# Optimization experiments

Measured on AMD Instinct MI355X. Metric: run time of the kernel, lower is better.

The kernel has to match this reference:

```python
import jax, jax.numpy as jnp
import numpy as np

ENTITY_SIZE = 100000
RELATION_SIZE = 500
DIM = 128
BATCH = 8192
MARGIN = 1.0


def _xavier_normal(key, shape):
    fan_in, fan_out = shape[1], shape[0]
    std = float(np.sqrt(2.0 / (fan_in + fan_out)))
    return jax.random.normal(key, shape, dtype=jnp.float32) * std


def setup_inputs() -> dict:
    key = jax.random.key(0)
    k1, k2, k3, k4, k5 = jax.random.split(key, 5)
    entities = _xavier_normal(k1, (ENTITY_SIZE, DIM))
    relations = _xavier_normal(k2, (RELATION_SIZE, DIM))
    transfer_matrix = _xavier_normal(k3, (RELATION_SIZE, DIM * DIM))
    positive_triples = jax.random.randint(k4, (BATCH, 3), 0, RELATION_SIZE, dtype=jnp.int32).astype(jnp.int64)
    negative_triples = jax.random.randint(k5, (BATCH, 3), 0, RELATION_SIZE, dtype=jnp.int32).astype(jnp.int64)
    return {
        "positive_triples": positive_triples,
        "negative_triples": negative_triples,
        "entities": entities,
        "relations": relations,
        "transfer_matrix": transfer_matrix,
    }


def _l2_normalize(x, eps=1e-12):
    # matches F.normalize(x, 2, -1): x / max(||x||_2, eps)
    n = jnp.linalg.norm(x, ord=2, axis=-1, keepdims=True)
    return x / jnp.maximum(n, eps)


def _calc_score(triples, entities, relations, transfer_matrix):
    heads, rels, tails = triples[:, 0], triples[:, 1], triples[:, 2]
    h = entities[heads]                      # [B, D]
    r = relations[rels]                      # [B, D]
    t = entities[tails]                      # [B, D]
    Mr = transfer_matrix[rels].reshape(-1, DIM, DIM)  # [B, D, D]
    # per-relation transfer: row-vector times matrix
    h = jnp.einsum('bd,bde->be', h, Mr)
    t = jnp.einsum('bd,bde->be', t, Mr)
    h = _l2_normalize(h)
    r = _l2_normalize(r)
    t = _l2_normalize(t)
    return jnp.sum(jnp.abs(h + r - t), axis=-1)  # L1 norm per triple, [B]


def reference(positive_triples, negative_triples, entities, relations, transfer_matrix):
    pos = _calc_score(positive_triples, entities, relations, transfer_matrix)
    neg = _calc_score(negative_triples, entities, relations, transfer_matrix)
    # MarginRankingLoss(margin=1.0) with target = -1:
    # mean(max(0, -y*(pos - neg) + margin)) = mean(relu(pos - neg + margin))
    return jnp.mean(jax.nn.relu(pos - neg + MARGIN))
```

## Files before the change

### kernel.cpp

```cpp
#include <hip/hip_runtime.h>
#include <math.h>

#define DIM 128
#define BATCH 8192
#define NTRIP (2 * BATCH)
#define NREL 500
#define MARGIN 1.0f
#define CAP 96
#define BSTR 136

typedef __attribute__((ext_vector_type(8))) short short8;
typedef __attribute__((ext_vector_type(4))) short short4v;
typedef __attribute__((ext_vector_type(4))) float f32x4;

__device__ __forceinline__ float wave_sum(float v) {
    v += __shfl_xor(v, 32, 64);
    v += __shfl_xor(v, 16, 64);
    v += __shfl_xor(v, 8, 64);
    v += __shfl_xor(v, 4, 64);
    v += __shfl_xor(v, 2, 64);
    v += __shfl_xor(v, 1, 64);
    return v;
}

__device__ __forceinline__ float quad_sum(float v) {
    v += __shfl_xor(v, 1, 64);
    v += __shfl_xor(v, 2, 64);
    v += __shfl_xor(v, 4, 64);
    v += __shfl_xor(v, 8, 64);
    return v;
}

__device__ __forceinline__ short f2bf(float f) {
    unsigned u = __float_as_uint(f);
    u = (u + 0x7fffu + ((u >> 16) & 1u)) >> 16;
    return (short)u;
}

__global__ __launch_bounds__(256)
void transr_bucket(const int* __restrict__ pos, const int* __restrict__ neg,
                   int* __restrict__ rel_count, int2* __restrict__ ht,
                   int* __restrict__ ids) {
    const int gid = blockIdx.x * 256 + threadIdx.x;
    const int* trip = (gid < BATCH) ? (pos + gid * 3) : (neg + (gid - BATCH) * 3);
    const int h = trip[0], r = trip[1], t = trip[2];
    const int slot = atomicAdd(&rel_count[r], 1);
    if (slot < CAP) {
        ht[r * CAP + slot] = make_int2(h, t);
        ids[r * CAP + slot] = gid;
    }
}

__global__ __launch_bounds__(512)
void transr_main(const float* __restrict__ entities,
                 const float* __restrict__ relations,
                 const float* __restrict__ transfer,
                 const int* __restrict__ rel_count,
                 const int2* __restrict__ ht, const int* __restrict__ ids,
                 float* __restrict__ scores) {
    __shared__ __align__(16) short Bt[DIM * BSTR];
    __shared__ float rhat_s[DIM];

    const int rel = blockIdx.x;
    const int tid = threadIdx.x;
    const int cnt = min(rel_count[rel], CAP);

    const int lane = tid & 63;
    const int w = tid >> 6;
    const int n = lane & 15;
    const int q = lane >> 4;
    const int jm = n >> 1;
    const int sel = n & 1;

    if (tid < DIM) rhat_s[tid] = relations[(size_t)rel * DIM + tid];

    const int2* __restrict__ ht_rel = ht + rel * CAP;
    const int* __restrict__ ids_rel = ids + rel * CAP;
    const int ntiles = (cnt + 7) >> 3;
    int2 pair0 = make_int2(0, 0);
    if (w < ntiles && cnt > 0) pair0 = ht_rel[min(w * 8 + jm, cnt - 1)];

    const float4* __restrict__ mrf4 = (const float4*)(transfer + (size_t)rel * (DIM * DIM));
    const int m = tid & 31;
    const int g = tid >> 5;
    const int n0 = m * 4;
#pragma unroll
    for (int it = 0; it < 2; ++it) {
        const int f0 = it * 2048 + g * 128 + m;
        const float4 v0 = mrf4[f0];
        const float4 v1 = mrf4[f0 + 32];
        const float4 v2 = mrf4[f0 + 64];
        const float4 v3 = mrf4[f0 + 96];
        const int k0 = it * 64 + g * 4;
        const float* p0 = (const float*)&v0;
        const float* p1 = (const float*)&v1;
        const float* p2 = (const float*)&v2;
        const float* p3 = (const float*)&v3;
#pragma unroll
        for (int j = 0; j < 4; ++j) {
            short4v wv;
            wv[0] = f2bf(p0[j]);
            wv[1] = f2bf(p1[j]);
            wv[2] = f2bf(p2[j]);
            wv[3] = f2bf(p3[j]);
            *(short4v*)(&Bt[(n0 + j) * BSTR + k0]) = wv;
        }
    }
    __syncthreads();

    const float a0 = rhat_s[lane], b0 = rhat_s[lane + 64];
    const float ssr = wave_sum(fmaf(a0, a0, b0 * b0));
    const float rinv = 1.0f / fmaxf(sqrtf(ssr), 1e-12f);

    float r_reg[8];
#pragma unroll
    for (int nt = 0; nt < 8; ++nt) r_reg[nt] = rhat_s[nt * 16 + n] * rinv;

    for (int tile = w; tile < ntiles; tile += 8) {
        const int2 pair = (tile == w) ? pair0 : ht_rel[min(tile * 8 + jm, cnt - 1)];
        const float* __restrict__ erow = entities + (size_t)(sel ? pair.y : pair.x) * DIM;

        short8 af[4];
#pragma unroll
        for (int kc = 0; kc < 4; ++kc) {
            const float4 u0 = *(const float4*)(erow + kc * 32 + q * 8);
            const float4 u1 = *(const float4*)(erow + kc * 32 + q * 8 + 4);
            short8 a;
            a[0] = f2bf(u0.x); a[1] = f2bf(u0.y); a[2] = f2bf(u0.z); a[3] = f2bf(u0.w);
            a[4] = f2bf(u1.x); a[5] = f2bf(u1.y); a[6] = f2bf(u1.z); a[7] = f2bf(u1.w);
            af[kc] = a;
        }

        f32x4 acc[8];
#pragma unroll
        for (int nt = 0; nt < 8; ++nt) acc[nt] = (f32x4){0.0f, 0.0f, 0.0f, 0.0f};
#pragma unroll
        for (int nt = 0; nt < 8; ++nt) {
            const short* __restrict__ bp = &Bt[(nt * 16 + n) * BSTR + q * 8];
#pragma unroll
            for (int kc = 0; kc < 4; ++kc) {
                const short8 bfr = *(const short8*)(bp + kc * 32);
                acc[nt] = __builtin_amdgcn_mfma_f32_16x16x32_bf16(af[kc], bfr, acc[nt], 0, 0, 0);
            }
        }

#pragma unroll
        for (int p = 0; p < 4; p += 2) {
            float hs = 0.0f, ts = 0.0f;
#pragma unroll
            for (int nt = 0; nt < 8; ++nt) {
                hs = fmaf(acc[nt][p], acc[nt][p], hs);
                ts = fmaf(acc[nt][p + 1], acc[nt][p + 1], ts);
            }
            hs = quad_sum(hs);
            ts = quad_sum(ts);
            const float invh = 1.0f / fmaxf(sqrtf(hs), 1e-12f);
            const float invt = 1.0f / fmaxf(sqrtf(ts), 1e-12f);
            float ss = 0.0f;
#pragma unroll
            for (int nt = 0; nt < 8; ++nt)
                ss += fabsf(fmaf(acc[nt][p], invh, r_reg[nt]) - acc[nt][p + 1] * invt);
            ss = quad_sum(ss);
            if (n == 0) {
                const int jS = min(tile * 8 + (q * 2 + (p >> 1)), cnt - 1);
                scores[ids_rel[jS]] = ss;
            }
        }
    }
}

__global__ __launch_bounds__(512)
void transr_loss(const float* __restrict__ scores, float* __restrict__ out) {
    const int tid = threadIdx.x;
    float s = 0.0f;
#pragma unroll
    for (int it = 0; it < 4; ++it) {
        const int i = it * 512 + tid;
        const float4 a = ((const float4*)scores)[i];
        const float4 b = ((const float4*)(scores + BATCH))[i];
        float d;
        d = a.x - b.x + MARGIN; s += (d > 0.0f) ? d : 0.0f;
        d = a.y - b.y + MARGIN; s += (d > 0.0f) ? d : 0.0f;
        d = a.z - b.z + MARGIN; s += (d > 0.0f) ? d : 0.0f;
        d = a.w - b.w + MARGIN; s += (d > 0.0f) ? d : 0.0f;
    }
    s = wave_sum(s);
    __shared__ float red[8];
    if ((tid & 63) == 0) red[tid >> 6] = s;
    __syncthreads();
    if (tid == 0) {
        float t = 0.0f;
#pragma unroll
        for (int i = 0; i < 8; ++i) t += red[i];
        out[0] = t * (1.0f / (float)BATCH);
    }
}

extern "C" void kernel_launch(void* const* d_in, const int* in_sizes, int n_in,
                              void* d_out, int out_size, void* d_ws, size_t ws_size,
                              hipStream_t stream) {
    const int*   pos       = (const int*)d_in[0];
    const int*   neg       = (const int*)d_in[1];
    const float* entities  = (const float*)d_in[2];
    const float* relations = (const float*)d_in[3];
    const float* transfer  = (const float*)d_in[4];
    float* out = (float*)d_out;

    int*   wsi       = (int*)d_ws;
    float* scores    = (float*)d_ws;
    int*   rel_count = wsi + 16384;
    int*   ids       = wsi + 16896;
    int2*  ht        = (int2*)(wsi + 65536);

    hipMemsetAsync(rel_count, 0, NREL * sizeof(int), stream);
    transr_bucket<<<NTRIP / 256, 256, 0, stream>>>(pos, neg, rel_count, ht, ids);
    transr_main<<<NREL, 512, 0, stream>>>(entities, relations, transfer, rel_count,
                                          ht, ids, scores);
    transr_loss<<<1, 512, 0, stream>>>(scores, out);
}
```

Before: 124.7 us.

## Fuse relation bucketing into main kernel and swizzle transfer-matrix LDS layout

Drops the memset and the separate bucket kernel. Each relation block now scans all 16384 triples itself and gathers its matching head/tail/id lists into shared memory with LDS atomics. The transposed transfer matrix in LDS moves from a padded stride to an XOR-swizzled unpadded layout to avoid bank conflicts. This removes two launches and global atomics, but every block redundantly reads all triple indices (about 200 KB per block, served mostly from L2).

```diff
diff --git a/kernel.cpp b/kernel.cpp
--- a/kernel.cpp
+++ b/kernel.cpp
@@ -6,8 +6,7 @@
 #define NTRIP (2 * BATCH)
 #define NREL 500
 #define MARGIN 1.0f
-#define CAP 96
-#define BSTR 136
+#define CAPL 128
 
 typedef __attribute__((ext_vector_type(8))) short short8;
 typedef __attribute__((ext_vector_type(4))) short short4v;
@@ -37,34 +36,19 @@
     return (short)u;
 }
 
-__global__ __launch_bounds__(256)
-void transr_bucket(const int* __restrict__ pos, const int* __restrict__ neg,
-                   int* __restrict__ rel_count, int2* __restrict__ ht,
-                   int* __restrict__ ids) {
-    const int gid = blockIdx.x * 256 + threadIdx.x;
-    const int* trip = (gid < BATCH) ? (pos + gid * 3) : (neg + (gid - BATCH) * 3);
-    const int h = trip[0], r = trip[1], t = trip[2];
-    const int slot = atomicAdd(&rel_count[r], 1);
-    if (slot < CAP) {
-        ht[r * CAP + slot] = make_int2(h, t);
-        ids[r * CAP + slot] = gid;
-    }
-}
-
 __global__ __launch_bounds__(512)
-void transr_main(const float* __restrict__ entities,
+void transr_main(const int* __restrict__ pos, const int* __restrict__ neg,
+                 const float* __restrict__ entities,
                  const float* __restrict__ relations,
                  const float* __restrict__ transfer,
-                 const int* __restrict__ rel_count,
-                 const int2* __restrict__ ht, const int* __restrict__ ids,
                  float* __restrict__ scores) {
-    __shared__ __align__(16) short Bt[DIM * BSTR];
+    __shared__ __align__(16) short Bt[DIM * DIM];
     __shared__ float rhat_s[DIM];
+    __shared__ int lh[CAPL], lt[CAPL], lid[CAPL];
+    __shared__ int lcnt;
 
     const int rel = blockIdx.x;
     const int tid = threadIdx.x;
-    const int cnt = min(rel_count[rel], CAP);
-
     const int lane = tid & 63;
     const int w = tid >> 6;
     const int n = lane & 15;
@@ -72,13 +56,9 @@
     const int jm = n >> 1;
     const int sel = n & 1;
 
+    if (tid == 0) lcnt = 0;
     if (tid < DIM) rhat_s[tid] = relations[(size_t)rel * DIM + tid];
-
-    const int2* __restrict__ ht_rel = ht + rel * CAP;
-    const int* __restrict__ ids_rel = ids + rel * CAP;
-    const int ntiles = (cnt + 7) >> 3;
-    int2 pair0 = make_int2(0, 0);
-    if (w < ntiles && cnt > 0) pair0 = ht_rel[min(w * 8 + jm, cnt - 1)];
+    __syncthreads();
 
     const float4* __restrict__ mrf4 = (const float4*)(transfer + (size_t)rel * (DIM * DIM));
     const int m = tid & 31;
@@ -92,21 +72,42 @@
         const float4 v2 = mrf4[f0 + 64];
         const float4 v3 = mrf4[f0 + 96];
         const int k0 = it * 64 + g * 4;
+        const int u = k0 >> 3;
+        const int klo = k0 & 7;
         const float* p0 = (const float*)&v0;
         const float* p1 = (const float*)&v1;
         const float* p2 = (const float*)&v2;
         const float* p3 = (const float*)&v3;
 #pragma unroll
         for (int j = 0; j < 4; ++j) {
+            const int col = n0 + j;
             short4v wv;
             wv[0] = f2bf(p0[j]);
             wv[1] = f2bf(p1[j]);
             wv[2] = f2bf(p2[j]);
             wv[3] = f2bf(p3[j]);
-            *(short4v*)(&Bt[(n0 + j) * BSTR + k0]) = wv;
+            const int up = u ^ ((col >> 1) & 7);
+            *(short4v*)(&Bt[col * DIM + up * 8 + klo]) = wv;
+        }
+    }
+
+#pragma unroll 4
+    for (int it = 0; it < 32; ++it) {
+        const int gid = it * 512 + tid;
+        const int* __restrict__ t3 =
+            (it < 16) ? (pos + gid * 3) : (neg + (gid - BATCH) * 3);
+        const int h = t3[0];
+        const int r = t3[1];
+        const int t = t3[2];
+        if (r == rel) {
+            const int s = atomicAdd(&lcnt, 1);
+            if (s < CAPL) { lh[s] = h; lt[s] = t; lid[s] = gid; }
         }
     }
     __syncthreads();
+
+    const int cnt = min(lcnt, CAPL);
+    if (cnt == 0) return;
 
     const float a0 = rhat_s[lane], b0 = rhat_s[lane + 64];
     const float ssr = wave_sum(fmaf(a0, a0, b0 * b0));
@@ -116,9 +117,12 @@
 #pragma unroll
     for (int nt = 0; nt < 8; ++nt) r_reg[nt] = rhat_s[nt * 16 + n] * rinv;
 
+    const int ntiles = (cnt + 7) >> 3;
+    const int fcol = n >> 1;
     for (int tile = w; tile < ntiles; tile += 8) {
-        const int2 pair = (tile == w) ? pair0 : ht_rel[min(tile * 8 + jm, cnt - 1)];
-        const float* __restrict__ erow = entities + (size_t)(sel ? pair.y : pair.x) * DIM;
+        const int j = min(tile * 8 + jm, cnt - 1);
+        const int eid = sel ? lt[j] : lh[j];
+        const float* __restrict__ erow = entities + (size_t)eid * DIM;
 
         short8 af[4];
 #pragma unroll
@@ -136,10 +140,10 @@
         for (int nt = 0; nt < 8; ++nt) acc[nt] = (f32x4){0.0f, 0.0f, 0.0f, 0.0f};
 #pragma unroll
         for (int nt = 0; nt < 8; ++nt) {
-            const short* __restrict__ bp = &Bt[(nt * 16 + n) * BSTR + q * 8];
+            const short* __restrict__ bp = &Bt[(nt * 16 + n) * DIM];
 #pragma unroll
             for (int kc = 0; kc < 4; ++kc) {
-                const short8 bfr = *(const short8*)(bp + kc * 32);
+                const short8 bfr = *(const short8*)(bp + (((kc * 4 + q) ^ fcol) << 3));
                 acc[nt] = __builtin_amdgcn_mfma_f32_16x16x32_bf16(af[kc], bfr, acc[nt], 0, 0, 0);
             }
         }
@@ -163,7 +167,7 @@
             ss = quad_sum(ss);
             if (n == 0) {
                 const int jS = min(tile * 8 + (q * 2 + (p >> 1)), cnt - 1);
-                scores[ids_rel[jS]] = ss;
+                scores[lid[jS]] = ss;
             }
         }
     }
@@ -206,15 +210,9 @@
     const float* transfer  = (const float*)d_in[4];
     float* out = (float*)d_out;
 
-    int*   wsi       = (int*)d_ws;
-    float* scores    = (float*)d_ws;
-    int*   rel_count = wsi + 16384;
-    int*   ids       = wsi + 16896;
-    int2*  ht        = (int2*)(wsi + 65536);
-
-    hipMemsetAsync(rel_count, 0, NREL * sizeof(int), stream);
-    transr_bucket<<<NTRIP / 256, 256, 0, stream>>>(pos, neg, rel_count, ht, ids);
-    transr_main<<<NREL, 512, 0, stream>>>(entities, relations, transfer, rel_count,
-                                          ht, ids, scores);
+    float* scores = (float*)d_ws;
+
+    transr_main<<<NREL, 512, 0, stream>>>(pos, neg, entities, relations, transfer,
+                                          scores);
     transr_loss<<<1, 512, 0, stream>>>(scores, out);
 }
```

Result: slower. 134.5 us (+7.8%).

## Fuse loss reduction into main kernel, swizzle LDS B tile, hoist first entity load

Applied to the files above, without the earlier changes.

The final margin-loss reduction moves into the main kernel: the last block, found through an atomic done counter, computes the mean, which removes a separate launch. The padded LDS layout for the transfer matrix becomes an XOR-swizzled unpadded layout to avoid bank conflicts and save LDS. The first tile's entity rows are loaded before the barrier so the loads overlap with staging the B matrix. Launch bounds now request 4 blocks per CU, which may force register spills.

```diff
diff --git a/kernel.cpp b/kernel.cpp
--- a/kernel.cpp
+++ b/kernel.cpp
@@ -7,7 +7,6 @@
 #define NREL 500
 #define MARGIN 1.0f
 #define CAP 96
-#define BSTR 136
 
 typedef __attribute__((ext_vector_type(8))) short short8;
 typedef __attribute__((ext_vector_type(4))) short short4v;
@@ -51,15 +50,18 @@
     }
 }
 
-__global__ __launch_bounds__(512)
+__global__ __launch_bounds__(512, 4)
 void transr_main(const float* __restrict__ entities,
                  const float* __restrict__ relations,
                  const float* __restrict__ transfer,
                  const int* __restrict__ rel_count,
                  const int2* __restrict__ ht, const int* __restrict__ ids,
-                 float* __restrict__ scores) {
-    __shared__ __align__(16) short Bt[DIM * BSTR];
+                 float* __restrict__ scores, int* __restrict__ done,
+                 float* __restrict__ out) {
+    __shared__ __align__(16) short Bt[DIM * DIM];
     __shared__ float rhat_s[DIM];
+    __shared__ float red[8];
+    __shared__ int is_last;
 
     const int rel = blockIdx.x;
     const int tid = threadIdx.x;
@@ -92,107 +94,140 @@
         const float4 v2 = mrf4[f0 + 64];
         const float4 v3 = mrf4[f0 + 96];
         const int k0 = it * 64 + g * 4;
+        const int u = k0 >> 3;
+        const int klo = k0 & 7;
         const float* p0 = (const float*)&v0;
         const float* p1 = (const float*)&v1;
         const float* p2 = (const float*)&v2;
         const float* p3 = (const float*)&v3;
 #pragma unroll
         for (int j = 0; j < 4; ++j) {
+            const int col = n0 + j;
             short4v wv;
             wv[0] = f2bf(p0[j]);
             wv[1] = f2bf(p1[j]);
             wv[2] = f2bf(p2[j]);
             wv[3] = f2bf(p3[j]);
-            *(short4v*)(&Bt[(n0 + j) * BSTR + k0]) = wv;
-        }
-    }
-    __syncthreads();
-
-    const float a0 = rhat_s[lane], b0 = rhat_s[lane + 64];
-    const float ssr = wave_sum(fmaf(a0, a0, b0 * b0));
-    const float rinv = 1.0f / fmaxf(sqrtf(ssr), 1e-12f);
-
-    float r_reg[8];
-#pragma unroll
-    for (int nt = 0; nt < 8; ++nt) r_reg[nt] = rhat_s[nt * 16 + n] * rinv;
-
-    for (int tile = w; tile < ntiles; tile += 8) {
-        const int2 pair = (tile == w) ? pair0 : ht_rel[min(tile * 8 + jm, cnt - 1)];
-        const float* __restrict__ erow = entities + (size_t)(sel ? pair.y : pair.x) * DIM;
-
-        short8 af[4];
+            const int up = u ^ ((col >> 1) & 7);
+            *(short4v*)(&Bt[col * DIM + up * 8 + klo]) = wv;
+        }
+    }
+
+    short8 af0[4];
+    {
+        const float* __restrict__ erow0 =
+            entities + (size_t)(sel ? pair0.y : pair0.x) * DIM;
 #pragma unroll
         for (int kc = 0; kc < 4; ++kc) {
-            const float4 u0 = *(const float4*)(erow + kc * 32 + q * 8);
-            const float4 u1 = *(const float4*)(erow + kc * 32 + q * 8 + 4);
+            const float4 u0 = *(const float4*)(erow0 + kc * 32 + q * 8);
+            const float4 u1 = *(const float4*)(erow0 + kc * 32 + q * 8 + 4);
             short8 a;
             a[0] = f2bf(u0.x); a[1] = f2bf(u0.y); a[2] = f2bf(u0.z); a[3] = f2bf(u0.w);
             a[4] = f2bf(u1.x); a[5] = f2bf(u1.y); a[6] = f2bf(u1.z); a[7] = f2bf(u1.w);
-            af[kc] = a;
-        }
-
-        f32x4 acc[8];
-#pragma unroll
-        for (int nt = 0; nt < 8; ++nt) acc[nt] = (f32x4){0.0f, 0.0f, 0.0f, 0.0f};
-#pragma unroll
-        for (int nt = 0; nt < 8; ++nt) {
-            const short* __restrict__ bp = &Bt[(nt * 16 + n) * BSTR + q * 8];
-#pragma unroll
-            for (int kc = 0; kc < 4; ++kc) {
-                const short8 bfr = *(const short8*)(bp + kc * 32);
-                acc[nt] = __builtin_amdgcn_mfma_f32_16x16x32_bf16(af[kc], bfr, acc[nt], 0, 0, 0);
+            af0[kc] = a;
+        }
+    }
+    __syncthreads();
+
+    if (cnt > 0) {
+        const float a0 = rhat_s[lane], b0 = rhat_s[lane + 64];
+        const float ssr = wave_sum(fmaf(a0, a0, b0 * b0));
+        const float rinv = 1.0f / fmaxf(sqrtf(ssr), 1e-12f);
+
+        float r_reg[8];
+#pragma unroll
+        for (int nt = 0; nt < 8; ++nt) r_reg[nt] = rhat_s[nt * 16 + n] * rinv;
+
+        const int fcol = n >> 1;
+        for (int tile = w; tile < ntiles; tile += 8) {
+            short8 af[4];
+            if (tile == w) {
+#pragma unroll
+                for (int kc = 0; kc < 4; ++kc) af[kc] = af0[kc];
+            } else {
+                const int j = min(tile * 8 + jm, cnt - 1);
+                const int2 pair = ht_rel[j];
+                const float* __restrict__ erow =
+                    entities + (size_t)(sel ? pair.y : pair.x) * DIM;
+#pragma unroll
+                for (int kc = 0; kc < 4; ++kc) {
+                    const float4 u0 = *(const float4*)(erow + kc * 32 + q * 8);
+                    const float4 u1 = *(const float4*)(erow + kc * 32 + q * 8 + 4);
+                    short8 a;
+                    a[0] = f2bf(u0.x); a[1] = f2bf(u0.y); a[2] = f2bf(u0.z); a[3] = f2bf(u0.w);
+                    a[4] = f2bf(u1.x); a[5] = f2bf(u1.y); a[6] = f2bf(u1.z); a[7] = f2bf(u1.w);
+                    af[kc] = a;
+                }
             }
-        }
-
-#pragma unroll
-        for (int p = 0; p < 4; p += 2) {
-            float hs = 0.0f, ts = 0.0f;
+
+            f32x4 acc[8];
+#pragma unroll
+            for (int nt = 0; nt < 8; ++nt) acc[nt] = (f32x4){0.0f, 0.0f, 0.0f, 0.0f};
 #pragma unroll
             for (int nt = 0; nt < 8; ++nt) {
-                hs = fmaf(acc[nt][p], acc[nt][p], hs);
-                ts = fmaf(acc[nt][p + 1], acc[nt][p + 1], ts);
+                const short* __restrict__ bp = &Bt[(nt * 16 + n) * DIM];
+#pragma unroll
+                for (int kc = 0; kc < 4; ++kc) {
+                    const short8 bfr = *(const short8*)(bp + (((kc * 4 + q) ^ fcol) << 3));
+                    acc[nt] = __builtin_amdgcn_mfma_f32_16x16x32_bf16(af[kc], bfr, acc[nt], 0, 0, 0);
+                }
             }
-            hs = quad_sum(hs);
-            ts = quad_sum(ts);
-            const float invh = 1.0f / fmaxf(sqrtf(hs), 1e-12f);
-            const float invt = 1.0f / fmaxf(sqrtf(ts), 1e-12f);
-            float ss = 0.0f;
-#pragma unroll
-            for (int nt = 0; nt < 8; ++nt)
-                ss += fabsf(fmaf(acc[nt][p], invh, r_reg[nt]) - acc[nt][p + 1] * invt);
-            ss = quad_sum(ss);
-            if (n == 0) {
-                const int jS = min(tile * 8 + (q * 2 + (p >> 1)), cnt - 1);
-                scores[ids_rel[jS]] = ss;
+
+#pragma unroll
+            for (int p = 0; p < 4; p += 2) {
+                float hs = 0.0f, ts = 0.0f;
+#pragma unroll
+                for (int nt = 0; nt < 8; ++nt) {
+                    hs = fmaf(acc[nt][p], acc[nt][p], hs);
+                    ts = fmaf(acc[nt][p + 1], acc[nt][p + 1], ts);
+                }
+                hs = quad_sum(hs);
+                ts = quad_sum(ts);
+                const float invh = 1.0f / fmaxf(sqrtf(hs), 1e-12f);
+                const float invt = 1.0f / fmaxf(sqrtf(ts), 1e-12f);
+                float ss = 0.0f;
+#pragma unroll
+                for (int nt = 0; nt < 8; ++nt)
+                    ss += fabsf(fmaf(acc[nt][p], invh, r_reg[nt]) - acc[nt][p + 1] * invt);
+                ss = quad_sum(ss);
+                if (n == 0) {
+                    const int jS = min(tile * 8 + (q * 2 + (p >> 1)), cnt - 1);
+                    scores[ids_rel[jS]] = ss;
+                }
             }
         }
     }
-}
-
-__global__ __launch_bounds__(512)
-void transr_loss(const float* __restrict__ scores, float* __restrict__ out) {
-    const int tid = threadIdx.x;
-    float s = 0.0f;
-#pragma unroll
-    for (int it = 0; it < 4; ++it) {
-        const int i = it * 512 + tid;
-        const float4 a = ((const float4*)scores)[i];
-        const float4 b = ((const float4*)(scores + BATCH))[i];
-        float d;
-        d = a.x - b.x + MARGIN; s += (d > 0.0f) ? d : 0.0f;
-        d = a.y - b.y + MARGIN; s += (d > 0.0f) ? d : 0.0f;
-        d = a.z - b.z + MARGIN; s += (d > 0.0f) ? d : 0.0f;
-        d = a.w - b.w + MARGIN; s += (d > 0.0f) ? d : 0.0f;
-    }
-    s = wave_sum(s);
-    __shared__ float red[8];
-    if ((tid & 63) == 0) red[tid >> 6] = s;
+
     __syncthreads();
     if (tid == 0) {
-        float t = 0.0f;
-#pragma unroll
-        for (int i = 0; i < 8; ++i) t += red[i];
-        out[0] = t * (1.0f / (float)BATCH);
+        const int prev = __hip_atomic_fetch_add(done, 1, __ATOMIC_ACQ_REL,
+                                                __HIP_MEMORY_SCOPE_AGENT);
+        is_last = (prev == NREL - 1) ? 1 : 0;
+    }
+    __syncthreads();
+    if (is_last) {
+        __threadfence();
+        float s = 0.0f;
+#pragma unroll
+        for (int it = 0; it < 4; ++it) {
+            const int i = it * 512 + tid;
+            const float4 a = ((const float4*)scores)[i];
+            const float4 b = ((const float4*)(scores + BATCH))[i];
+            float d;
+            d = a.x - b.x + MARGIN; s += (d > 0.0f) ? d : 0.0f;
+            d = a.y - b.y + MARGIN; s += (d > 0.0f) ? d : 0.0f;
+            d = a.z - b.z + MARGIN; s += (d > 0.0f) ? d : 0.0f;
+            d = a.w - b.w + MARGIN; s += (d > 0.0f) ? d : 0.0f;
+        }
+        s = wave_sum(s);
+        if ((tid & 63) == 0) red[tid >> 6] = s;
+        __syncthreads();
+        if (tid == 0) {
+            float t = 0.0f;
+#pragma unroll
+            for (int i = 0; i < 8; ++i) t += red[i];
+            out[0] = t * (1.0f / (float)BATCH);
+        }
     }
 }
 
@@ -209,12 +244,12 @@
     int*   wsi       = (int*)d_ws;
     float* scores    = (float*)d_ws;
     int*   rel_count = wsi + 16384;
+    int*   done      = wsi + 16884;
     int*   ids       = wsi + 16896;
     int2*  ht        = (int2*)(wsi + 65536);
 
-    hipMemsetAsync(rel_count, 0, NREL * sizeof(int), stream);
+    (void)hipMemsetAsync(rel_count, 0, (NREL + 1) * sizeof(int), stream);
     transr_bucket<<<NTRIP / 256, 256, 0, stream>>>(pos, neg, rel_count, ht, ids);
     transr_main<<<NREL, 512, 0, stream>>>(entities, relations, transfer, rel_count,
-                                          ht, ids, scores);
-    transr_loss<<<1, 512, 0, stream>>>(scores, out);
-}
+                                          ht, ids, scores, done, out);
+}
```

Result: slower. 162.0 us (+29.9%).
